# Kernel tuning notes

Measured on AMD Instinct MI355X. Metric: run time of the kernel, lower is better.

## Reference

```python
import jax, jax.numpy as jnp
import numpy as np

INV_SIGMA = 10.0
EPS = 1e-8  # torch CosineSimilarity default eps


def setup_inputs() -> dict:
    key = jax.random.key(0)
    k1, k2, k3, k4 = jax.random.split(key, 4)
    n, C, G, N = 16384, 32, 128, 200000
    x = jax.random.normal(k1, (n, G), dtype=jnp.float32)
    v = jax.random.normal(k2, (n, G), dtype=jnp.float32)
    k = jax.random.randint(k3, (n, C), 0, N, dtype=jnp.int64)
    X = jax.random.normal(k4, (N, G), dtype=jnp.float32)
    return {"x": x, "v": v, "k": k, "X": X}


def reference(x, v, k, X):
    # gather neighbors: [n, C, G]
    deltas = X[k] - x[:, None, :]
    # cosine similarity along dim=2 (torch clamps norm product at eps)
    num = jnp.einsum('ng,ncg->nc', v, deltas)
    v_norm = jnp.linalg.norm(v, axis=-1)          # [n]
    d_norm = jnp.linalg.norm(deltas, axis=-1)     # [n, C]
    cs = num / jnp.maximum(v_norm[:, None] * d_norm, EPS)
    # expm1 scaling + L1-style normalization over neighbors
    Tv = jnp.expm1(cs * INV_SIGMA)
    Tv = Tv / jnp.abs(Tv).sum(axis=1, keepdims=True)
    # NaN mask on dX (same gather as deltas)
    dX = jnp.nan_to_num(deltas, nan=0.0)
    subtractor = Tv.mean(axis=1, keepdims=True) * dX.sum(axis=1)  # [n,1]*[n,G]
    v_proj = jnp.einsum('ncg,nc->ng', dX, Tv) - subtractor
    return v_proj
```

## Files before the change

### kernel.cpp

```cpp
#include <hip/hip_runtime.h>
#include <math.h>

#define GDIM 128
#define CDIM 32
#define EPSV 1e-8f
#define INV_SIGMA 10.0f
#define PAD 4

__global__ __launch_bounds__(256, 8) void nc_kernel(
    const float* __restrict__ x, const float* __restrict__ v,
    const int*   __restrict__ k, const float* __restrict__ X,
    float* __restrict__ out)
{
    const int i = blockIdx.x;
    const int t = threadIdx.x;

    __shared__ float sdel[CDIM][GDIM + PAD];
    __shared__ float sv[GDIM];
    __shared__ float stv[CDIM];
    __shared__ float s_vnorm;
    __shared__ float s_mean;

    float va = 0.f, vb = 0.f;
    if (t < 64) {
        va = v[(size_t)i * GDIM + t];
        vb = v[(size_t)i * GDIM + t + 64];
    }

    const int lane4 = (t & 31) * 4;
    const int cbase = t >> 5;
    int k0 = k[(size_t)i * CDIM + cbase];
    int k1 = k[(size_t)i * CDIM + cbase + 8];
    int k2 = k[(size_t)i * CDIM + cbase + 16];
    int k3 = k[(size_t)i * CDIM + cbase + 24];
    const float4 xv = *reinterpret_cast<const float4*>(&x[(size_t)i * GDIM + lane4]);
    const float4 X0 = *reinterpret_cast<const float4*>(&X[(size_t)k0 * GDIM + lane4]);
    const float4 X1 = *reinterpret_cast<const float4*>(&X[(size_t)k1 * GDIM + lane4]);
    const float4 X2 = *reinterpret_cast<const float4*>(&X[(size_t)k2 * GDIM + lane4]);
    const float4 X3 = *reinterpret_cast<const float4*>(&X[(size_t)k3 * GDIM + lane4]);

    if (t < 64) {
        sv[t] = va; sv[t + 64] = vb;
        float vn = va * va + vb * vb;
        #pragma unroll
        for (int off = 32; off; off >>= 1) vn += __shfl_xor(vn, off);
        if (t == 0) s_vnorm = sqrtf(vn);
    }

    {
        float4 d;
        d.x = X0.x - xv.x; d.y = X0.y - xv.y; d.z = X0.z - xv.z; d.w = X0.w - xv.w;
        *reinterpret_cast<float4*>(&sdel[cbase][lane4]) = d;
        d.x = X1.x - xv.x; d.y = X1.y - xv.y; d.z = X1.z - xv.z; d.w = X1.w - xv.w;
        *reinterpret_cast<float4*>(&sdel[cbase + 8][lane4]) = d;
        d.x = X2.x - xv.x; d.y = X2.y - xv.y; d.z = X2.z - xv.z; d.w = X2.w - xv.w;
        *reinterpret_cast<float4*>(&sdel[cbase + 16][lane4]) = d;
        d.x = X3.x - xv.x; d.y = X3.y - xv.y; d.z = X3.z - xv.z; d.w = X3.w - xv.w;
        *reinterpret_cast<float4*>(&sdel[cbase + 24][lane4]) = d;
    }
    __syncthreads();

    {
        const int c = t >> 3;
        const int l = t & 7;
        float num = 0.f, ss = 0.f;
        #pragma unroll
        for (int j = 0; j < 16; ++j) {
            const int g = l + 8 * j;
            const float d = sdel[c][g];
            num = fmaf(sv[g], d, num);
            ss  = fmaf(d, d, ss);
        }
        #pragma unroll
        for (int off = 4; off; off >>= 1) {
            num += __shfl_xor(num, off);
            ss  += __shfl_xor(ss, off);
        }
        if (l == 0) {
            const float dn = sqrtf(ss);
            const float cs = num / fmaxf(s_vnorm * dn, EPSV);
            stv[c] = expm1f(cs * INV_SIGMA);
        }
    }
    __syncthreads();

    if (t < CDIM) {
        const float tv = stv[t];
        float sa = fabsf(tv), st = tv;
        #pragma unroll
        for (int off = 16; off; off >>= 1) {
            sa += __shfl_xor(sa, off);
            st += __shfl_xor(st, off);
        }
        stv[t] = tv / sa;
        if (t == 0) s_mean = (st / sa) * (1.0f / CDIM);
    }
    __syncthreads();

    if (t < GDIM) {
        const int g = t;
        float acc = 0.f, sd = 0.f;
        #pragma unroll
        for (int c = 0; c < CDIM; ++c) {
            const float d = sdel[c][g];
            acc = fmaf(d, stv[c], acc);
            sd += d;
        }
        out[(size_t)i * GDIM + g] = acc - s_mean * sd;
    }
}

extern "C" void kernel_launch(void* const* d_in, const int* in_sizes, int n_in,
                              void* d_out, int out_size, void* d_ws, size_t ws_size,
                              hipStream_t stream) {
    const float* x = (const float*)d_in[0];
    const float* v = (const float*)d_in[1];
    const int*   k = (const int*)  d_in[2];
    const float* X = (const float*)d_in[3];
    float* out = (float*)d_out;
    const int n = in_sizes[0] / GDIM;
    nc_kernel<<<n, 256, 0, stream>>>(x, v, k, X, out);
}
```

Baseline: 179.2 us.

## Process eight rows per block with register-prefetched gathers of the next row

Each block now handles eight rows in sequence. While the current row is being processed, the gathered neighbor rows of X and the x and v rows for the next row are loaded into registers, so global gather latency is hidden behind compute. The normalization step is folded into the final output loop, which removes a barrier phase, and the syncthreads calls are replaced with raw barriers plus explicit waits. The costs are a grid reduced to n/8 blocks, which lowers parallelism, higher register pressure, and barrier handling that is fragile around shared-memory reuse.

```diff
diff --git a/kernel.cpp b/kernel.cpp
--- a/kernel.cpp
+++ b/kernel.cpp
@@ -3,6 +3,7 @@
 
 #define GDIM 128
 #define CDIM 32
+#define ROWS 8
 #define EPSV 1e-8f
 #define INV_SIGMA 10.0f
 #define PAD 4
@@ -12,101 +13,118 @@
     const int*   __restrict__ k, const float* __restrict__ X,
     float* __restrict__ out)
 {
-    const int i = blockIdx.x;
-    const int t = threadIdx.x;
+    const int  t  = threadIdx.x;
+    const long i0 = (long)blockIdx.x * ROWS;
 
     __shared__ float sdel[CDIM][GDIM + PAD];
-    __shared__ float sv[GDIM];
+    __shared__ float sv[2][GDIM];
+    __shared__ float svn[2];
     __shared__ float stv[CDIM];
-    __shared__ float s_vnorm;
-    __shared__ float s_mean;
+    __shared__ int   sk[ROWS * CDIM];
 
-    float va = 0.f, vb = 0.f;
-    if (t < 64) {
-        va = v[(size_t)i * GDIM + t];
-        vb = v[(size_t)i * GDIM + t + 64];
-    }
+    sk[t] = k[i0 * CDIM + t];
+    asm volatile("s_waitcnt lgkmcnt(0)" ::: "memory");
+    __builtin_amdgcn_s_barrier();
 
     const int lane4 = (t & 31) * 4;
     const int cbase = t >> 5;
-    int k0 = k[(size_t)i * CDIM + cbase];
-    int k1 = k[(size_t)i * CDIM + cbase + 8];
-    int k2 = k[(size_t)i * CDIM + cbase + 16];
-    int k3 = k[(size_t)i * CDIM + cbase + 24];
-    const float4 xv = *reinterpret_cast<const float4*>(&x[(size_t)i * GDIM + lane4]);
-    const float4 X0 = *reinterpret_cast<const float4*>(&X[(size_t)k0 * GDIM + lane4]);
-    const float4 X1 = *reinterpret_cast<const float4*>(&X[(size_t)k1 * GDIM + lane4]);
-    const float4 X2 = *reinterpret_cast<const float4*>(&X[(size_t)k2 * GDIM + lane4]);
-    const float4 X3 = *reinterpret_cast<const float4*>(&X[(size_t)k3 * GDIM + lane4]);
 
-    if (t < 64) {
-        sv[t] = va; sv[t + 64] = vb;
-        float vn = va * va + vb * vb;
-        #pragma unroll
-        for (int off = 32; off; off >>= 1) vn += __shfl_xor(vn, off);
-        if (t == 0) s_vnorm = sqrtf(vn);
+    float4 X0, X1, X2, X3, xv;
+    float  va = 0.f, vb = 0.f;
+    {
+        const int b = cbase;
+        X0 = *(const float4*)&X[(size_t)sk[b     ] * GDIM + lane4];
+        X1 = *(const float4*)&X[(size_t)sk[b +  8] * GDIM + lane4];
+        X2 = *(const float4*)&X[(size_t)sk[b + 16] * GDIM + lane4];
+        X3 = *(const float4*)&X[(size_t)sk[b + 24] * GDIM + lane4];
+        xv = *(const float4*)&x[(size_t)i0 * GDIM + lane4];
+        if (t < 64) {
+            va = v[(size_t)i0 * GDIM + t];
+            vb = v[(size_t)i0 * GDIM + t + 64];
+        }
     }
 
-    {
-        float4 d;
-        d.x = X0.x - xv.x; d.y = X0.y - xv.y; d.z = X0.z - xv.z; d.w = X0.w - xv.w;
-        *reinterpret_cast<float4*>(&sdel[cbase][lane4]) = d;
-        d.x = X1.x - xv.x; d.y = X1.y - xv.y; d.z = X1.z - xv.z; d.w = X1.w - xv.w;
-        *reinterpret_cast<float4*>(&sdel[cbase + 8][lane4]) = d;
-        d.x = X2.x - xv.x; d.y = X2.y - xv.y; d.z = X2.z - xv.z; d.w = X2.w - xv.w;
-        *reinterpret_cast<float4*>(&sdel[cbase + 16][lane4]) = d;
-        d.x = X3.x - xv.x; d.y = X3.y - xv.y; d.z = X3.z - xv.z; d.w = X3.w - xv.w;
-        *reinterpret_cast<float4*>(&sdel[cbase + 24][lane4]) = d;
-    }
-    __syncthreads();
+    #pragma unroll
+    for (int j = 0; j < ROWS; ++j) {
+        const int p = j & 1;
 
-    {
-        const int c = t >> 3;
-        const int l = t & 7;
-        float num = 0.f, ss = 0.f;
-        #pragma unroll
-        for (int j = 0; j < 16; ++j) {
-            const int g = l + 8 * j;
-            const float d = sdel[c][g];
-            num = fmaf(sv[g], d, num);
-            ss  = fmaf(d, d, ss);
+        __builtin_amdgcn_s_barrier();
+
+        {
+            float4 d;
+            d.x = X0.x - xv.x; d.y = X0.y - xv.y; d.z = X0.z - xv.z; d.w = X0.w - xv.w;
+            *(float4*)&sdel[cbase][lane4] = d;
+            d.x = X1.x - xv.x; d.y = X1.y - xv.y; d.z = X1.z - xv.z; d.w = X1.w - xv.w;
+            *(float4*)&sdel[cbase + 8][lane4] = d;
+            d.x = X2.x - xv.x; d.y = X2.y - xv.y; d.z = X2.z - xv.z; d.w = X2.w - xv.w;
+            *(float4*)&sdel[cbase + 16][lane4] = d;
+            d.x = X3.x - xv.x; d.y = X3.y - xv.y; d.z = X3.z - xv.z; d.w = X3.w - xv.w;
+            *(float4*)&sdel[cbase + 24][lane4] = d;
         }
-        #pragma unroll
-        for (int off = 4; off; off >>= 1) {
-            num += __shfl_xor(num, off);
-            ss  += __shfl_xor(ss, off);
+        if (t < 64) {
+            sv[p][t] = va; sv[p][t + 64] = vb;
+            float vn = va * va + vb * vb;
+            #pragma unroll
+            for (int off = 32; off; off >>= 1) vn += __shfl_xor(vn, off);
+            if (t == 0) svn[p] = sqrtf(vn);
         }
-        if (l == 0) {
-            const float dn = sqrtf(ss);
-            const float cs = num / fmaxf(s_vnorm * dn, EPSV);
-            stv[c] = expm1f(cs * INV_SIGMA);
+
+        if (j + 1 < ROWS) {
+            const int b = (j + 1) * CDIM + cbase;
+            const long in = i0 + j + 1;
+            X0 = *(const float4*)&X[(size_t)sk[b     ] * GDIM + lane4];
+            X1 = *(const float4*)&X[(size_t)sk[b +  8] * GDIM + lane4];
+            X2 = *(const float4*)&X[(size_t)sk[b + 16] * GDIM + lane4];
+            X3 = *(const float4*)&X[(size_t)sk[b + 24] * GDIM + lane4];
+            xv = *(const float4*)&x[(size_t)in * GDIM + lane4];
+            if (t < 64) {
+                va = v[(size_t)in * GDIM + t];
+                vb = v[(size_t)in * GDIM + t + 64];
+            }
         }
-    }
-    __syncthreads();
+        __builtin_amdgcn_sched_barrier(0);
 
-    if (t < CDIM) {
-        const float tv = stv[t];
-        float sa = fabsf(tv), st = tv;
-        #pragma unroll
-        for (int off = 16; off; off >>= 1) {
-            sa += __shfl_xor(sa, off);
-            st += __shfl_xor(st, off);
+        asm volatile("s_waitcnt lgkmcnt(0)" ::: "memory");
+        __builtin_amdgcn_s_barrier();
+
+        {
+            const int c = t >> 3;
+            const int l = t & 7;
+            float num = 0.f, ss = 0.f;
+            #pragma unroll
+            for (int q = 0; q < 16; ++q) {
+                const int g = l + 8 * q;
+                const float d = sdel[c][g];
+                num = fmaf(sv[p][g], d, num);
+                ss  = fmaf(d, d, ss);
+            }
+            #pragma unroll
+            for (int off = 4; off; off >>= 1) {
+                num += __shfl_xor(num, off);
+                ss  += __shfl_xor(ss, off);
+            }
+            if (l == 0) {
+                const float dn = sqrtf(ss);
+                const float cs = num / fmaxf(svn[p] * dn, EPSV);
+                stv[c] = expm1f(cs * INV_SIGMA);
+            }
         }
-        stv[t] = tv / sa;
-        if (t == 0) s_mean = (st / sa) * (1.0f / CDIM);
-    }
-    __syncthreads();
+        asm volatile("s_waitcnt lgkmcnt(0)" ::: "memory");
+        __builtin_amdgcn_s_barrier();
 
-    if (t < GDIM) {
-        const int g = t;
-        float acc = 0.f, sd = 0.f;
-        #pragma unroll
-        for (int c = 0; c < CDIM; ++c) {
-            const float d = sdel[c][g];
-            acc = fmaf(d, stv[c], acc);
-            sd += d;
+        if (t < GDIM) {
+            float acc = 0.f, sd = 0.f, sa = 0.f, st = 0.f;
+            #pragma unroll
+            for (int c = 0; c < CDIM; ++c) {
+                const float tvc = stv[c];
+                const float d   = sdel[c][t];
+                acc = fmaf(d, tvc, acc);
+                sd += d;
+                sa += fabsf(tvc);
+                st += tvc;
+            }
+            out[(size_t)(i0 + j) * GDIM + t] = (acc - (st * (1.0f / CDIM)) * sd) / sa;
         }
-        out[(size_t)i * GDIM + g] = acc - s_mean * sd;
     }
 }
 
@@ -119,5 +137,5 @@
     const float* X = (const float*)d_in[3];
     float* out = (float*)d_out;
     const int n = in_sizes[0] / GDIM;
-    nc_kernel<<<n, 256, 0, stream>>>(x, v, k, X, out);
+    nc_kernel<<<n / ROWS, 256, 0, stream>>>(x, v, k, X, out);
 }
```

Result: slower. 191.9 us (+7.1%).

## Process one row per wavefront with register accumulation, dropping shared memory

Applied to the files above, without the earlier changes.

Each wavefront now handles one output row. The two half-waves each gather alternate neighbor rows as float4 loads. Cosine similarity, expm1 weighting and the weighted and plain sums are done in registers, using shuffle reductions. The final normalization is applied once at the end, which removes the shared-memory staging and the three block barriers. The trade-offs are 16 serial dependent gather iterations per wave, each with shuffle reductions, and launch_bounds no longer requesting 8 blocks per CU.

```diff
diff --git a/kernel.cpp b/kernel.cpp
--- a/kernel.cpp
+++ b/kernel.cpp
@@ -5,108 +5,79 @@
 #define CDIM 32
 #define EPSV 1e-8f
 #define INV_SIGMA 10.0f
-#define PAD 4
 
-__global__ __launch_bounds__(256, 8) void nc_kernel(
+__global__ __launch_bounds__(256) void nc_kernel(
     const float* __restrict__ x, const float* __restrict__ v,
     const int*   __restrict__ k, const float* __restrict__ X,
     float* __restrict__ out)
 {
-    const int i = blockIdx.x;
-    const int t = threadIdx.x;
+    const int t    = threadIdx.x;
+    const int wave = t >> 6;
+    const int lane = t & 63;
+    const int m    = lane & 31;
+    const int h    = lane >> 5;
+    const long i   = (long)blockIdx.x * 4 + wave;
 
-    __shared__ float sdel[CDIM][GDIM + PAD];
-    __shared__ float sv[GDIM];
-    __shared__ float stv[CDIM];
-    __shared__ float s_vnorm;
-    __shared__ float s_mean;
+    const float4 xv = *reinterpret_cast<const float4*>(&x[i * GDIM + m * 4]);
+    const float4 vv = *reinterpret_cast<const float4*>(&v[i * GDIM + m * 4]);
 
-    float va = 0.f, vb = 0.f;
-    if (t < 64) {
-        va = v[(size_t)i * GDIM + t];
-        vb = v[(size_t)i * GDIM + t + 64];
-    }
+    float vn = vv.x * vv.x + vv.y * vv.y + vv.z * vv.z + vv.w * vv.w;
+    #pragma unroll
+    for (int off = 16; off; off >>= 1) vn += __shfl_xor(vn, off);
+    const float vnorm = sqrtf(vn);
 
-    const int lane4 = (t & 31) * 4;
-    const int cbase = t >> 5;
-    int k0 = k[(size_t)i * CDIM + cbase];
-    int k1 = k[(size_t)i * CDIM + cbase + 8];
-    int k2 = k[(size_t)i * CDIM + cbase + 16];
-    int k3 = k[(size_t)i * CDIM + cbase + 24];
-    const float4 xv = *reinterpret_cast<const float4*>(&x[(size_t)i * GDIM + lane4]);
-    const float4 X0 = *reinterpret_cast<const float4*>(&X[(size_t)k0 * GDIM + lane4]);
-    const float4 X1 = *reinterpret_cast<const float4*>(&X[(size_t)k1 * GDIM + lane4]);
-    const float4 X2 = *reinterpret_cast<const float4*>(&X[(size_t)k2 * GDIM + lane4]);
-    const float4 X3 = *reinterpret_cast<const float4*>(&X[(size_t)k3 * GDIM + lane4]);
+    const int kk = k[i * CDIM + m];
 
-    if (t < 64) {
-        sv[t] = va; sv[t + 64] = vb;
-        float vn = va * va + vb * vb;
+    float4 A = make_float4(0.f, 0.f, 0.f, 0.f);
+    float4 S = make_float4(0.f, 0.f, 0.f, 0.f);
+    float  sa = 0.f, st = 0.f;
+
+    #pragma unroll
+    for (int it = 0; it < 16; ++it) {
+        const int ke = __shfl(kk, 2 * it);
+        const int ko = __shfl(kk, 2 * it + 1);
+        const int kc = h ? ko : ke;
+
+        const float4 Xr = *reinterpret_cast<const float4*>(
+            &X[(size_t)kc * GDIM + m * 4]);
+        float4 d;
+        d.x = Xr.x - xv.x; d.y = Xr.y - xv.y;
+        d.z = Xr.z - xv.z; d.w = Xr.w - xv.w;
+
+        float num = vv.x * d.x + vv.y * d.y + vv.z * d.z + vv.w * d.w;
+        float ss  = d.x * d.x + d.y * d.y + d.z * d.z + d.w * d.w;
         #pragma unroll
-        for (int off = 32; off; off >>= 1) vn += __shfl_xor(vn, off);
-        if (t == 0) s_vnorm = sqrtf(vn);
-    }
-
-    {
-        float4 d;
-        d.x = X0.x - xv.x; d.y = X0.y - xv.y; d.z = X0.z - xv.z; d.w = X0.w - xv.w;
-        *reinterpret_cast<float4*>(&sdel[cbase][lane4]) = d;
-        d.x = X1.x - xv.x; d.y = X1.y - xv.y; d.z = X1.z - xv.z; d.w = X1.w - xv.w;
-        *reinterpret_cast<float4*>(&sdel[cbase + 8][lane4]) = d;
-        d.x = X2.x - xv.x; d.y = X2.y - xv.y; d.z = X2.z - xv.z; d.w = X2.w - xv.w;
-        *reinterpret_cast<float4*>(&sdel[cbase + 16][lane4]) = d;
-        d.x = X3.x - xv.x; d.y = X3.y - xv.y; d.z = X3.z - xv.z; d.w = X3.w - xv.w;
-        *reinterpret_cast<float4*>(&sdel[cbase + 24][lane4]) = d;
-    }
-    __syncthreads();
-
-    {
-        const int c = t >> 3;
-        const int l = t & 7;
-        float num = 0.f, ss = 0.f;
-        #pragma unroll
-        for (int j = 0; j < 16; ++j) {
-            const int g = l + 8 * j;
-            const float d = sdel[c][g];
-            num = fmaf(sv[g], d, num);
-            ss  = fmaf(d, d, ss);
-        }
-        #pragma unroll
-        for (int off = 4; off; off >>= 1) {
+        for (int off = 16; off; off >>= 1) {
             num += __shfl_xor(num, off);
             ss  += __shfl_xor(ss, off);
         }
-        if (l == 0) {
-            const float dn = sqrtf(ss);
-            const float cs = num / fmaxf(s_vnorm * dn, EPSV);
-            stv[c] = expm1f(cs * INV_SIGMA);
-        }
+
+        const float cs = num / fmaxf(vnorm * sqrtf(ss), EPSV);
+        const float tv = expm1f(cs * INV_SIGMA);
+        sa += fabsf(tv);
+        st += tv;
+
+        A.x = fmaf(tv, d.x, A.x); A.y = fmaf(tv, d.y, A.y);
+        A.z = fmaf(tv, d.z, A.z); A.w = fmaf(tv, d.w, A.w);
+        S.x += d.x; S.y += d.y; S.z += d.z; S.w += d.w;
     }
-    __syncthreads();
 
-    if (t < CDIM) {
-        const float tv = stv[t];
-        float sa = fabsf(tv), st = tv;
-        #pragma unroll
-        for (int off = 16; off; off >>= 1) {
-            sa += __shfl_xor(sa, off);
-            st += __shfl_xor(st, off);
-        }
-        stv[t] = tv / sa;
-        if (t == 0) s_mean = (st / sa) * (1.0f / CDIM);
-    }
-    __syncthreads();
+    sa += __shfl_xor(sa, 32);
+    st += __shfl_xor(st, 32);
+    A.x += __shfl_xor(A.x, 32); A.y += __shfl_xor(A.y, 32);
+    A.z += __shfl_xor(A.z, 32); A.w += __shfl_xor(A.w, 32);
+    S.x += __shfl_xor(S.x, 32); S.y += __shfl_xor(S.y, 32);
+    S.z += __shfl_xor(S.z, 32); S.w += __shfl_xor(S.w, 32);
 
-    if (t < GDIM) {
-        const int g = t;
-        float acc = 0.f, sd = 0.f;
-        #pragma unroll
-        for (int c = 0; c < CDIM; ++c) {
-            const float d = sdel[c][g];
-            acc = fmaf(d, stv[c], acc);
-            sd += d;
-        }
-        out[(size_t)i * GDIM + g] = acc - s_mean * sd;
+    if (h == 0) {
+        const float scale = 1.0f / sa;
+        const float mst   = st * (1.0f / CDIM);
+        float4 o;
+        o.x = (A.x - mst * S.x) * scale;
+        o.y = (A.y - mst * S.y) * scale;
+        o.z = (A.z - mst * S.z) * scale;
+        o.w = (A.w - mst * S.w) * scale;
+        *reinterpret_cast<float4*>(&out[i * GDIM + m * 4]) = o;
     }
 }
 
@@ -119,5 +90,5 @@
     const float* X = (const float*)d_in[3];
     float* out = (float*)d_out;
     const int n = in_sizes[0] / GDIM;
-    nc_kernel<<<n, 256, 0, stream>>>(x, v, k, X, out);
+    nc_kernel<<<n / 4, 256, 0, stream>>>(x, v, k, X, out);
 }
```

Result: slower. 188.1 us (+5.0%).
